# Kernel tuning notes

Measured on AMD Instinct MI355X. Metric: run time of the kernel, lower is better.

## Reference

```python
import jax, jax.numpy as jnp
import numpy as np


def _idct_tables():
    steps = jnp.arange(8, dtype=jnp.float32) / 16.0
    f = 2.0 * jnp.arange(8, dtype=jnp.float32) + 1.0
    h = jnp.cos(jnp.outer(steps, f * jnp.pi))            # [u, x]
    # basis[x, y, u, v] = h[u, x] * h[v, y]
    basis = h.T[:, None, :, None] * h.T[None, :, None, :]
    c = jnp.ones(8, dtype=jnp.float32).at[0].set(jnp.sqrt(jnp.float32(0.5)))
    scale = 0.25 * jnp.outer(c, c)                        # [u, v]
    return basis, scale


def setup_inputs() -> dict:
    key = jax.random.key(0)
    dct = jax.random.normal(key, (16, 64, 256, 256), dtype=jnp.float32)
    mean = jnp.zeros(64, dtype=jnp.float32)
    std = jnp.ones(64, dtype=jnp.float32)
    return {"dct": dct, "mean": mean, "std": std}


def reference(dct, mean, std):
    B, C, H, W = dct.shape  # C == 64
    basis, scale = _idct_tables()
    # destandardize per DCT coefficient
    d = dct * std[None, :, None, None] + mean[None, :, None, None]
    d = d.reshape(B, 8, 8, H, W)  # (B, u, v, H, W)
    # 2D IDCT: sum over u, v of scale[u,v] * basis[x,y,u,v] * d[b,u,v,h,w]
    # (mathematically equal to the original's broadcasted outer-product sum)
    res = jnp.einsum('uv,xyuv,buvhw->bxyhw', scale, basis, d)
    # interleave block pixels into full image: (B, H, x, W, y) -> (B, 1, 8H, 8W)
    res = jnp.transpose(res, (0, 3, 1, 4, 2)).reshape(B, 1, 8 * H, 8 * W)
    return (res + 128.0) / 255.0
```

## Files before the change

### kernel.cpp

```cpp
#include <hip/hip_runtime.h>

__device__ __constant__ float G[64] = {
    0.3535533906f,  0.3535533906f,  0.3535533906f,  0.3535533906f,
    0.3535533906f,  0.3535533906f,  0.3535533906f,  0.3535533906f,

    0.4903926402f,  0.4157348062f,  0.2777851165f,  0.0975451610f,
   -0.0975451610f, -0.2777851165f, -0.4157348062f, -0.4903926402f,

    0.4619397663f,  0.1913417162f, -0.1913417162f, -0.4619397663f,
   -0.4619397663f, -0.1913417162f,  0.1913417162f,  0.4619397663f,

    0.4157348062f, -0.0975451610f, -0.4903926402f, -0.2777851165f,
    0.2777851165f,  0.4903926402f,  0.0975451610f, -0.4157348062f,

    0.3535533906f, -0.3535533906f, -0.3535533906f,  0.3535533906f,
    0.3535533906f, -0.3535533906f, -0.3535533906f,  0.3535533906f,

    0.2777851165f, -0.4903926402f,  0.0975451610f,  0.4157348062f,
   -0.4157348062f, -0.0975451610f,  0.4903926402f, -0.2777851165f,

    0.1913417162f, -0.4619397663f,  0.4619397663f, -0.1913417162f,
   -0.1913417162f,  0.4619397663f, -0.4619397663f,  0.1913417162f,

    0.0975451610f, -0.2777851165f,  0.4157348062f, -0.4903926402f,
    0.4903926402f, -0.4157348062f,  0.2777851165f, -0.0975451610f,
};

__global__ __launch_bounds__(256) void idct_kernel(
    const float* __restrict__ dct,
    const float* __restrict__ mean_,
    const float* __restrict__ std_,
    float* __restrict__ out)
{
    const int gid = blockIdx.x * 256 + threadIdx.x;
    const int w = gid & 255;
    const int h = (gid >> 8) & 255;
    const int b = gid >> 16;

    const float* p = dct + (size_t)b * 64 * 65536 + (size_t)h * 256 + (size_t)w;

    float t[8][8];
#pragma unroll
    for (int x = 0; x < 8; ++x)
#pragma unroll
        for (int v = 0; v < 8; ++v) t[x][v] = 0.0f;

#pragma unroll
    for (int u = 0; u < 8; ++u) {
#pragma unroll
        for (int v = 0; v < 8; ++v) {
            const int c = u * 8 + v;
            const float raw = p[(size_t)c * 65536];
            const float dv = fmaf(raw, std_[c], mean_[c]);
#pragma unroll
            for (int x = 0; x < 8; ++x)
                t[x][v] = fmaf(G[u * 8 + x], dv, t[x][v]);
        }
    }

    const float inv255 = 1.0f / 255.0f;
    const float off128 = 128.0f / 255.0f;

    const size_t obase = (size_t)b * (2048u * 2048u) + (size_t)(h * 8) * 2048 + (size_t)(w * 8);

#pragma unroll
    for (int x = 0; x < 8; ++x) {
        float pix[8];
#pragma unroll
        for (int y = 0; y < 8; ++y) {
            float s = 0.0f;
#pragma unroll
            for (int v = 0; v < 8; ++v)
                s = fmaf(G[v * 8 + y], t[x][v], s);
            pix[y] = fmaf(s, inv255, off128);
        }
        float4* o = (float4*)(out + obase + (size_t)x * 2048);
        o[0] = make_float4(pix[0], pix[1], pix[2], pix[3]);
        o[1] = make_float4(pix[4], pix[5], pix[6], pix[7]);
    }
}

extern "C" void kernel_launch(void* const* d_in, const int* in_sizes, int n_in,
                              void* d_out, int out_size, void* d_ws, size_t ws_size,
                              hipStream_t stream) {
    const float* dct  = (const float*)d_in[0];
    const float* mean = (const float*)d_in[1];
    const float* std_ = (const float*)d_in[2];
    float* out = (float*)d_out;

    const int total_threads = 16 * 256 * 256;
    const int block = 256;
    const int grid = total_threads / block;
    idct_kernel<<<grid, block, 0, stream>>>(dct, mean, std_, out);
}
```

Baseline: 435.8 us.

## Stage DCT coefficients into LDS via direct global-to-LDS loads

Each workgroup now loads all 64 coefficient planes for one row (64x256 floats, 64KB) into LDS using global_load_lds 16-byte async copies. It then runs the first IDCT pass from LDS and writes the intermediate back into LDS, cutting per-thread register pressure from the 8x8 accumulator array. The goal is wider, more efficient global loads and higher occupancy, and the pass order is restructured to go through v then u. The cost is a 64KB LDS footprint per block, which limits how many blocks fit on a CU, plus an extra LDS round trip.

```diff
diff --git a/kernel.cpp b/kernel.cpp
--- a/kernel.cpp
+++ b/kernel.cpp
@@ -32,49 +32,67 @@
     const float* __restrict__ std_,
     float* __restrict__ out)
 {
-    const int gid = blockIdx.x * 256 + threadIdx.x;
-    const int w = gid & 255;
-    const int h = (gid >> 8) & 255;
-    const int b = gid >> 16;
+    __shared__ float lds[64 * 256];
 
-    const float* p = dct + (size_t)b * 64 * 65536 + (size_t)h * 256 + (size_t)w;
+    const int t    = threadIdx.x;
+    const int wg   = blockIdx.x;
+    const int h    = wg & 255;
+    const int b    = wg >> 8;
+    const int wave = t >> 6;
+    const int lane = t & 63;
 
-    float t[8][8];
-#pragma unroll
-    for (int x = 0; x < 8; ++x)
-#pragma unroll
-        for (int v = 0; v < 8; ++v) t[x][v] = 0.0f;
+    const float* gbase = dct + (size_t)b * 64u * 65536u + (size_t)h * 256u;
 
 #pragma unroll
-    for (int u = 0; u < 8; ++u) {
+    for (int i = 0; i < 16; ++i) {
+        const int c = wave * 16 + i;
+        const float* src = gbase + (size_t)c * 65536u + (size_t)lane * 4u;
+        __builtin_amdgcn_global_load_lds(
+            (const __attribute__((address_space(1))) void*)src,
+            (__attribute__((address_space(3))) void*)&lds[c * 256],
+            16, 0, 0);
+    }
+    __syncthreads();
+
 #pragma unroll
-        for (int v = 0; v < 8; ++v) {
+    for (int v = 0; v < 8; ++v) {
+        float dv[8];
+#pragma unroll
+        for (int u = 0; u < 8; ++u) {
             const int c = u * 8 + v;
-            const float raw = p[(size_t)c * 65536];
-            const float dv = fmaf(raw, std_[c], mean_[c]);
+            dv[u] = fmaf(lds[c * 256 + t], std_[c], mean_[c]);
+        }
 #pragma unroll
-            for (int x = 0; x < 8; ++x)
-                t[x][v] = fmaf(G[u * 8 + x], dv, t[x][v]);
+        for (int x = 0; x < 8; ++x) {
+            float s = 0.0f;
+#pragma unroll
+            for (int u = 0; u < 8; ++u)
+                s = fmaf(G[u * 8 + x], dv[u], s);
+            lds[(x * 8 + v) * 256 + t] = s;
         }
     }
 
     const float inv255 = 1.0f / 255.0f;
     const float off128 = 128.0f / 255.0f;
-
-    const size_t obase = (size_t)b * (2048u * 2048u) + (size_t)(h * 8) * 2048 + (size_t)(w * 8);
+    const size_t obase = (size_t)b * (2048u * 2048u)
+                       + (size_t)(h * 8) * 2048u + (size_t)t * 8u;
 
 #pragma unroll
     for (int x = 0; x < 8; ++x) {
+        float tv[8];
+#pragma unroll
+        for (int v = 0; v < 8; ++v)
+            tv[v] = lds[(x * 8 + v) * 256 + t];
         float pix[8];
 #pragma unroll
         for (int y = 0; y < 8; ++y) {
             float s = 0.0f;
 #pragma unroll
             for (int v = 0; v < 8; ++v)
-                s = fmaf(G[v * 8 + y], t[x][v], s);
+                s = fmaf(G[v * 8 + y], tv[v], s);
             pix[y] = fmaf(s, inv255, off128);
         }
-        float4* o = (float4*)(out + obase + (size_t)x * 2048);
+        float4* o = (float4*)(out + obase + (size_t)x * 2048u);
         o[0] = make_float4(pix[0], pix[1], pix[2], pix[3]);
         o[1] = make_float4(pix[4], pix[5], pix[6], pix[7]);
     }
@@ -88,8 +106,6 @@
     const float* std_ = (const float*)d_in[2];
     float* out = (float*)d_out;
 
-    const int total_threads = 16 * 256 * 256;
-    const int block = 256;
-    const int grid = total_threads / block;
-    idct_kernel<<<grid, block, 0, stream>>>(dct, mean, std_, out);
+    const int grid = 16 * 256;
+    idct_kernel<<<grid, 256, 0, stream>>>(dct, mean, std_, out);
 }
```

Measured after the change: 443.3 us. About the same (+1.7%).
